# Performance work log

Hardware: AMD Instinct MI355X
Metric: run time of the kernel (lower is better)

The kernel has to match this reference:

```python
import jax, jax.numpy as jnp
import numpy as np

B, T, H, DD, DS = 256, 365, 512, 32, 27  # batch, timesteps, units, num_dynamic, num_static


def setup_inputs() -> dict:
    key = jax.random.key(0)
    ks = jax.random.split(key, 6)
    scale = 0.05
    bias = jnp.zeros((3 * H,), jnp.float32).at[:H].add(1.0)  # unit forget bias on f-block
    return {
        "x_dyn": jax.random.normal(ks[0], (B, T, DD), jnp.float32),
        "x_static": jax.random.normal(ks[1], (B, DS), jnp.float32),
        "kernel": jax.random.normal(ks[2], (DD, 3 * H), jnp.float32) * scale,
        "recurrent_kernel": jax.random.normal(ks[3], (H, 3 * H), jnp.float32) * scale,
        "bias": bias,
        "static_kernel": jax.random.normal(ks[4], (DS, H), jnp.float32) * scale,
        "static_bias": jnp.zeros((H,), jnp.float32),
    }


def hard_sigmoid(x):
    return jnp.clip(0.2 * x + 0.5, 0.0, 1.0)


def reference(x_dyn, x_static, kernel, recurrent_kernel, bias, static_kernel, static_bias):
    Hn = static_bias.shape[0]
    # static input gate, constant across time: [B, H]
    i_gate = hard_sigmoid(x_static @ static_kernel + static_bias)
    # precompute input contribution for all timesteps: [T, B, 3H]
    zx = jnp.einsum('btd,dk->tbk', x_dyn, kernel) + bias

    def step(carry, z_t):
        h, c = carry
        z = z_t + h @ recurrent_kernel  # [B, 3H]
        f = hard_sigmoid(z[:, :Hn])
        g = jnp.tanh(z[:, Hn:2 * Hn])
        o = hard_sigmoid(z[:, 2 * Hn:])
        c = f * c + i_gate * g
        h = o * jnp.tanh(c)
        return (h, c), h

    b = x_dyn.shape[0]
    h0 = jnp.zeros((b, Hn), x_dyn.dtype)
    (_, _), hs = jax.lax.scan(step, (h0, h0), zx)
    return jnp.transpose(hs, (1, 0, 2))  # [B, T, H]
```

## Files before the change

### kernel.cpp

```cpp
#include <hip/hip_runtime.h>
#include <stdint.h>

#define TSTEPS 365
#define BATCH  256
#define HU     512
#define DDIM   32
#define DSTAT  27
#define KTOT   544
#define KPAD   552
#define NCOLS  96
#define ZPAD   20

typedef __attribute__((ext_vector_type(8))) short s8v;
typedef __attribute__((ext_vector_type(4))) float f4v;

__device__ __forceinline__ float b2f(uint16_t u) {
    union { uint32_t i; float f; } v; v.i = ((uint32_t)u) << 16; return v.f;
}
__device__ __forceinline__ uint16_t f2b(float f) {
    uint32_t x = __float_as_uint(f);
    uint32_t r = x + 0x7FFFu + ((x >> 16) & 1u);
    return (uint16_t)(r >> 16);
}
__device__ __forceinline__ float loadf(const void* p, long i, bool fp32) {
    return fp32 ? ((const float*)p)[i] : b2f(((const uint16_t*)p)[i]);
}
__device__ __forceinline__ bool detect_fp32(const void* bias) {
    return *((const uint32_t*)bias) == 0x3F800000u;
}
__device__ __forceinline__ float hsig(float x) {
    return fminf(fmaxf(0.2f * x + 0.5f, 0.0f), 1.0f);
}
__device__ __forceinline__ float tanh_fast(float x) {
    float e = __expf(2.0f * x);
    return 1.0f - 2.0f * __builtin_amdgcn_rcpf(e + 1.0f);
}
__device__ __forceinline__ uint32_t load_x_nt(const void* x, bool fp32, int b, int t, int d) {
    long i = ((long)b * TSTEPS + t) * DDIM + d;
    return fp32 ? __builtin_nontemporal_load(((const uint32_t*)x) + i)
                : (uint32_t)__builtin_nontemporal_load(((const uint16_t*)x) + i);
}
__device__ __forceinline__ float xval(uint32_t r, bool fp32) {
    return fp32 ? __uint_as_float(r) : b2f((uint16_t)r);
}

__global__ __launch_bounds__(256) void k_prep_w(
    const void* __restrict__ rk, const void* __restrict__ kin,
    const void* __restrict__ bias,
    uint16_t* __restrict__ Wc, float* __restrict__ biasf)
{
    bool fp32 = detect_fp32(bias);
    __shared__ float tile[32][33];
    int jt = blockIdx.x, kt = blockIdx.y;
    int c = threadIdx.x & 31, r0 = threadIdx.x >> 5;
    #pragma unroll
    for (int i = 0; i < 4; i++) {
        int r = r0 + 8 * i;
        int k = kt * 32 + r, j = jt * 32 + c;
        float v;
        if (k < HU) v = loadf(rk, (long)k * 1536 + j, fp32);
        else        v = loadf(kin, (long)(k - HU) * 1536 + j, fp32);
        tile[r][c] = v;
    }
    __syncthreads();
    #pragma unroll
    for (int i = 0; i < 4; i++) {
        int r = r0 + 8 * i;
        int j = jt * 32 + r, k = kt * 32 + c;
        Wc[(long)j * KTOT + k] = f2b(tile[c][r]);
    }
    if (jt == 0 && kt == 0)
        for (int idx = threadIdx.x; idx < 1536; idx += 256)
            biasf[idx] = loadf(bias, idx, fp32);
}

__global__ __launch_bounds__(256) void k_igate(
    const void* __restrict__ xs, const void* __restrict__ sk,
    const void* __restrict__ sbias, const void* __restrict__ bias,
    float* __restrict__ igate)
{
    bool fp32 = detect_fp32(bias);
    int b = blockIdx.x;
    for (int u = threadIdx.x; u < HU; u += 256) {
        float acc = loadf(sbias, u, fp32);
        #pragma unroll
        for (int d = 0; d < DSTAT; d++)
            acc += loadf(xs, (long)b * DSTAT + d, fp32) * loadf(sk, (long)d * HU + u, fp32);
        igate[(long)b * HU + u] = hsig(acc);
    }
}

__device__ __forceinline__ void unpack_h(uint64_t v, uint16_t* rowh, uint16_t* rowl, int u2) {
    uint32_t p0 = (uint32_t)v, p1 = (uint32_t)(v >> 32);
    *(uint32_t*)&rowh[u2] = (p0 >> 16) | (p1 & 0xFFFF0000u);
    *(uint32_t*)&rowl[u2] = (p0 & 0xFFFFu) | (p1 << 16);
}

__global__ __launch_bounds__(512) void k_persist(
    const void* __restrict__ xdyn, const void* __restrict__ bias,
    const uint16_t* __restrict__ Wc, const float* __restrict__ biasf,
    const float* __restrict__ igate,
    uint64_t* __restrict__ h0, uint64_t* __restrict__ h1,
    void* __restrict__ out)
{
    bool fp32 = detect_fp32(bias);
    __shared__ __align__(16) uint16_t ldsAh[16][KPAD];
    __shared__ __align__(16) uint16_t ldsAl[16][KPAD];
    __shared__ __align__(16) float    zbufP[2][NCOLS][ZPAD];

    int tid = threadIdx.x;
    int bg = blockIdx.x & 15;
    int ug = blockIdx.x >> 4;
    int wv = tid >> 6, lane = tid & 63;
    int n = lane & 15, q = lane >> 4;
    int gte = wv >> 1, hh = wv & 1;

    s8v wr0[9], wr1[9];
    float bz0 = 0.f, bz1 = 0.f;
    if (wv < 6) {
        int j0 = (gte << 9) + (ug << 5) + n;
        int j1 = j0 + 16;
        if (hh == 0) {
            #pragma unroll
            for (int kk = 0; kk < 9; kk++) {
                int k0 = kk * 32 + q * 8;
                wr0[kk] = *(const s8v*)(Wc + (long)j0 * KTOT + k0);
                wr1[kk] = *(const s8v*)(Wc + (long)j1 * KTOT + k0);
            }
            bz0 = biasf[j0];
            bz1 = biasf[j1];
        } else {
            #pragma unroll
            for (int kk = 0; kk < 8; kk++) {
                int k0 = (9 + kk) * 32 + q * 8;
                wr0[kk] = *(const s8v*)(Wc + (long)j0 * KTOT + k0);
                wr1[kk] = *(const s8v*)(Wc + (long)j1 * KTOT + k0);
            }
        }
    }

    int em = tid >> 5;
    int sl = tid & 31;
    int eb = bg * 16 + em;
    int ugb = ug << 5;
    float ig0 = igate[(long)eb * HU + ugb + sl];
    float c0r = 0.f;
    long rowbase = ((long)eb) << 8;

    for (int t = 0; t < TSTEPS; t++) {
        const uint64_t* Rp = (t & 1) ? h1 : h0;
        uint64_t*       Wp = (t & 1) ? h0 : h1;

        uint32_t xr0 = load_x_nt(xdyn, fp32, bg * 16 + em, t, sl);

        uint64_t hb[8];
        if (t == 0) {
            #pragma unroll
            for (int i = 0; i < 8; i++) hb[i] = 0ull;
        } else {
            uint32_t texp = (((uint32_t)(t - 1)) >> 1) & 1u;
            int guard = 0;
            for (;;) {
                #pragma unroll
                for (int i = 0; i < 8; i++)
                    hb[i] = __hip_atomic_load(&Rp[rowbase + i * 32 + sl],
                                              __ATOMIC_RELAXED, __HIP_MEMORY_SCOPE_AGENT);
                uint32_t bad = 0;
                #pragma unroll
                for (int i = 0; i < 8; i++)
                    bad |= ((uint32_t)hb[i] ^ texp) & 1u;
                if (__all((int)(bad == 0))) break;
                if (++guard > (1 << 20)) break;
                if (guard > 64) __builtin_amdgcn_s_sleep(1);
            }
            asm volatile("" ::: "memory");
        }
        #pragma unroll
        for (int i = 0; i < 8; i++)
            unpack_h(hb[i], ldsAh[em], ldsAl[em], 2 * (i * 32 + sl));

        {
            float v0 = xval(xr0, fp32);
            uint16_t a0 = f2b(v0);
            ldsAh[em][HU + sl] = a0;
            ldsAl[em][HU + sl] = f2b(v0 - b2f(a0));
        }
        __syncthreads();

        if (wv < 6) {
            f4v a0h, a1h;
            if (hh == 0) { a0h = (f4v){bz0, bz0, bz0, bz0}; a1h = (f4v){bz1, bz1, bz1, bz1}; }
            else         { a0h = (f4v){0.f, 0.f, 0.f, 0.f}; a1h = (f4v){0.f, 0.f, 0.f, 0.f}; }
            f4v a0l = {0.f, 0.f, 0.f, 0.f}, a1l = {0.f, 0.f, 0.f, 0.f};
            if (hh == 0) {
                #pragma unroll
                for (int kk = 0; kk < 9; kk++) {
                    int k0 = kk * 32 + q * 8;
                    s8v ah = *(const s8v*)&ldsAh[n][k0];
                    s8v al = *(const s8v*)&ldsAl[n][k0];
                    a0h = __builtin_amdgcn_mfma_f32_16x16x32_bf16(ah, wr0[kk], a0h, 0, 0, 0);
                    a1h = __builtin_amdgcn_mfma_f32_16x16x32_bf16(ah, wr1[kk], a1h, 0, 0, 0);
                    a0l = __builtin_amdgcn_mfma_f32_16x16x32_bf16(al, wr0[kk], a0l, 0, 0, 0);
                    a1l = __builtin_amdgcn_mfma_f32_16x16x32_bf16(al, wr1[kk], a1l, 0, 0, 0);
                }
            } else {
                #pragma unroll
                for (int kk = 0; kk < 8; kk++) {
                    int k0 = (9 + kk) * 32 + q * 8;
                    s8v ah = *(const s8v*)&ldsAh[n][k0];
                    s8v al = *(const s8v*)&ldsAl[n][k0];
                    a0h = __builtin_amdgcn_mfma_f32_16x16x32_bf16(ah, wr0[kk], a0h, 0, 0, 0);
                    a1h = __builtin_amdgcn_mfma_f32_16x16x32_bf16(ah, wr1[kk], a1h, 0, 0, 0);
                    a0l = __builtin_amdgcn_mfma_f32_16x16x32_bf16(al, wr0[kk], a0l, 0, 0, 0);
                    a1l = __builtin_amdgcn_mfma_f32_16x16x32_bf16(al, wr1[kk], a1l, 0, 0, 0);
                }
            }
            int ci0 = (gte << 5) + n, ci1 = ci0 + 16;
            *(f4v*)&zbufP[hh][ci0][q * 4] = a0h + a0l;
            *(f4v*)&zbufP[hh][ci1][q * 4] = a1h + a1l;
        }
        __syncthreads();

        {
            float zf = zbufP[0][sl][em]      + zbufP[1][sl][em];
            float zg = zbufP[0][32 + sl][em] + zbufP[1][32 + sl][em];
            float zo = zbufP[0][64 + sl][em] + zbufP[1][64 + sl][em];
            float f0 = hsig(zf);
            float g0 = tanh_fast(zg);
            float o0 = hsig(zo);
            c0r = f0 * c0r + ig0 * g0;
            float hv0 = o0 * tanh_fast(c0r);
            uint32_t tg = (((uint32_t)t) >> 1) & 1u;
            uint16_t hi0 = f2b(hv0);
            uint16_t lo0 = (uint16_t)((f2b(hv0 - b2f(hi0)) & 0xFFFEu) | tg);
            uint32_t me32 = ((uint32_t)hi0 << 16) | lo0;
            uint32_t nb32 = __shfl_down(me32, 1);
            if (!(sl & 1)) {
                uint64_t pk = ((uint64_t)nb32 << 32) | me32;
                __hip_atomic_store(&Wp[rowbase + (ugb >> 1) + (sl >> 1)], pk,
                                   __ATOMIC_RELAXED, __HIP_MEMORY_SCOPE_AGENT);
            }
            long oo = ((long)eb * TSTEPS + t) * HU + ugb + sl;
            if (fp32) {
                __builtin_nontemporal_store(hv0, &((float*)out)[oo]);
            } else if (!(sl & 1)) {
                __builtin_nontemporal_store(
                    (uint32_t)(hi0 | (nb32 & 0xFFFF0000u)), &((uint32_t*)out)[oo >> 1]);
            }
        }
    }
}

__global__ __launch_bounds__(256) void k_step_fb(
    const void* __restrict__ xdyn, const void* __restrict__ bias,
    const uint16_t* __restrict__ Wc, const float* __restrict__ biasf,
    const float* __restrict__ igate, float* __restrict__ c_fb,
    const uint64_t* __restrict__ Rp, uint64_t* __restrict__ Wp,
    void* __restrict__ out, int t)
{
    bool fp32 = detect_fp32(bias);
    __shared__ __align__(16) uint16_t ldsAh[16][KPAD];
    __shared__ __align__(16) uint16_t ldsAl[16][KPAD];
    __shared__ __align__(16) float    zbuf[NCOLS][ZPAD];

    int tid = threadIdx.x;
    int bg = blockIdx.x & 15;
    int ug = blockIdx.x >> 4;
    int w = tid >> 6, lane = tid & 63;
    int n = lane & 15, q = lane >> 4;
    int em = tid >> 4, ep = tid & 15;
    int u0 = 2 * ep, u1 = u0 + 1;
    int eb = bg * 16 + em;
    int ugb = ug << 5;

    long rowbase = ((long)eb) << 8;
    #pragma unroll 4
    for (int kb = 0; kb < 16; kb++)
        unpack_h((t == 0) ? 0ull : Rp[rowbase + kb * 16 + ep],
                 ldsAh[em], ldsAl[em], kb * 32 + 2 * ep);
    #pragma unroll
    for (int it = 0; it < 2; it++) {
        int e = tid + it * 256;
        int m = e >> 5, d = e & 31;
        float v = loadf(xdyn, ((long)(bg * 16 + m) * TSTEPS + t) * DDIM + d, fp32);
        uint16_t hi = f2b(v);
        ldsAh[m][HU + d] = hi;
        ldsAl[m][HU + d] = f2b(v - b2f(hi));
    }
    __syncthreads();

    if (w < 3) {
        int j0 = (w << 9) + (ug << 5) + n;
        int j1 = j0 + 16;
        float bz0 = biasf[j0], bz1 = biasf[j1];
        f4v a0h = {bz0, bz0, bz0, bz0}, a0l = {0.f, 0.f, 0.f, 0.f};
        f4v a1h = {bz1, bz1, bz1, bz1}, a1l = {0.f, 0.f, 0.f, 0.f};
        #pragma unroll
        for (int kt = 0; kt < 17; kt++) {
            int k0 = kt * 32 + q * 8;
            s8v b0 = *(const s8v*)(Wc + (long)j0 * KTOT + k0);
            s8v b1 = *(const s8v*)(Wc + (long)j1 * KTOT + k0);
            s8v ah = *(const s8v*)&ldsAh[n][k0];
            s8v al = *(const s8v*)&ldsAl[n][k0];
            a0h = __builtin_amdgcn_mfma_f32_16x16x32_bf16(ah, b0, a0h, 0, 0, 0);
            a1h = __builtin_amdgcn_mfma_f32_16x16x32_bf16(ah, b1, a1h, 0, 0, 0);
            a0l = __builtin_amdgcn_mfma_f32_16x16x32_bf16(al, b0, a0l, 0, 0, 0);
            a1l = __builtin_amdgcn_mfma_f32_16x16x32_bf16(al, b1, a1l, 0, 0, 0);
        }
        int ci0 = 32 * w + n, ci1 = ci0 + 16;
        *(f4v*)&zbuf[ci0][q * 4] = a0h + a0l;
        *(f4v*)&zbuf[ci1][q * 4] = a1h + a1l;
    }
    __syncthreads();

    {
        float f0 = hsig(zbuf[u0][em]);
        float g0 = tanhf(zbuf[32 + u0][em]);
        float o0 = hsig(zbuf[64 + u0][em]);
        float f1 = hsig(zbuf[u1][em]);
        float g1 = tanhf(zbuf[32 + u1][em]);
        float o1 = hsig(zbuf[64 + u1][em]);
        float2* cp = (float2*)&c_fb[((long)eb << 9) + ugb + u0];
        float2 cv = *cp;
        cv.x = f0 * cv.x + igate[(long)eb * HU + ugb + u0] * g0;
        cv.y = f1 * cv.y + igate[(long)eb * HU + ugb + u1] * g1;
        *cp = cv;
        float hv0 = o0 * tanhf(cv.x);
        float hv1 = o1 * tanhf(cv.y);
        uint16_t hi0 = f2b(hv0), lo0 = f2b(hv0 - b2f(hi0));
        uint16_t hi1 = f2b(hv1), lo1 = f2b(hv1 - b2f(hi1));
        Wp[((long)eb << 8) + (ugb >> 1) + ep] =
            ((uint64_t)(((uint32_t)hi1 << 16) | lo1) << 32) | (((uint32_t)hi0 << 16) | lo0);
        long oo = ((long)eb * TSTEPS + t) * HU + ugb + u0;
        if (fp32) {
            ((float*)out)[oo] = hv0;
            ((float*)out)[oo + 1] = hv1;
        } else {
            ((uint32_t*)out)[oo >> 1] = hi0 | ((uint32_t)hi1 << 16);
        }
    }
}

extern "C" void kernel_launch(void* const* d_in, const int* in_sizes, int n_in,
                              void* d_out, int out_size, void* d_ws, size_t ws_size,
                              hipStream_t stream) {
    const void* xdyn  = d_in[0];
    const void* xstat = d_in[1];
    const void* kin   = d_in[2];
    const void* rk    = d_in[3];
    const void* bias  = d_in[4];
    const void* sk    = d_in[5];
    const void* sbias = d_in[6];

    char* w = (char*)d_ws;
    size_t off = 0;
    uint16_t* Wc = (uint16_t*)(w + off);  off += (size_t)1536 * KTOT * 2;
    float* biasf = (float*)(w + off);     off += 1536 * 4;
    float* igate = (float*)(w + off);     off += (size_t)BATCH * HU * 4;
    size_t hs = off;
    uint64_t* h0 = (uint64_t*)(w + off);  off += (size_t)BATCH * HU * 2 * 2;
    uint64_t* h1 = (uint64_t*)(w + off);  off += (size_t)BATCH * HU * 2 * 2;
    size_t he = off;
    float* c_fb  = (float*)(w + off);     off += (size_t)BATCH * HU * 4;

    hipMemsetAsync(w + hs, 0x01, he - hs, stream);
    hipMemsetAsync(w + he, 0, off - he, stream);

    k_prep_w<<<dim3(48, 17), 256, 0, stream>>>(rk, kin, bias, Wc, biasf);
    k_igate<<<dim3(256), 256, 0, stream>>>(xstat, sk, sbias, bias, igate);

    void* args[] = {
        (void*)&xdyn, (void*)&bias, (void*)&Wc, (void*)&biasf, (void*)&igate,
        (void*)&h0, (void*)&h1, (void*)&d_out
    };
    hipError_t err = hipLaunchCooperativeKernel((void*)k_persist, dim3(256), dim3(512),
                                                args, 0, stream);
    if (err != hipSuccess) {
        for (int t = 0; t < TSTEPS; t++) {
            const uint64_t* Rp = (t & 1) ? h1 : h0;
            uint64_t* Wp = (t & 1) ? h0 : h1;
            k_step_fb<<<dim3(256), 256, 0, stream>>>(xdyn, bias, Wc, biasf, igate,
                                                     c_fb, Rp, Wp, d_out, t);
        }
    }
    (void)ws_size; (void)n_in; (void)out_size; (void)in_sizes;
}
```

Baseline: 1.105 ms.

## Double block size to 1024 threads, splitting MFMA columns across twice the waves

The persistent LSTM kernel now launches 1024-thread blocks. Each of 12 waves computes one 16-column MFMA tile instead of two, which halves the serial MFMA chain per wave. The h-vector polling load is spread over all 16 waves, so each lane reads 4 words instead of 8. The cost is more waves contending in each __syncthreads, only half the threads doing the elementwise update, and a tighter register budget under launch_bounds(1024).

```diff
diff --git a/kernel.cpp b/kernel.cpp
--- a/kernel.cpp
+++ b/kernel.cpp
@@ -96,7 +96,7 @@
     *(uint32_t*)&rowl[u2] = (p0 & 0xFFFFu) | (p1 << 16);
 }
 
-__global__ __launch_bounds__(512) void k_persist(
+__global__ __launch_bounds__(1024, 4) void k_persist(
     const void* __restrict__ xdyn, const void* __restrict__ bias,
     const uint16_t* __restrict__ Wc, const float* __restrict__ biasf,
     const float* __restrict__ igate,
@@ -113,61 +113,56 @@
     int ug = blockIdx.x >> 4;
     int wv = tid >> 6, lane = tid & 63;
     int n = lane & 15, q = lane >> 4;
-    int gte = wv >> 1, hh = wv & 1;
-
-    s8v wr0[9], wr1[9];
-    float bz0 = 0.f, bz1 = 0.f;
-    if (wv < 6) {
-        int j0 = (gte << 9) + (ug << 5) + n;
-        int j1 = j0 + 16;
+    int gte = wv >> 2, hh = (wv >> 1) & 1, js = wv & 1;
+
+    s8v wr0[9];
+    float bz0 = 0.f;
+    if (wv < 12) {
+        int j0 = (gte << 9) + (ug << 5) + (js << 4) + n;
         if (hh == 0) {
             #pragma unroll
-            for (int kk = 0; kk < 9; kk++) {
-                int k0 = kk * 32 + q * 8;
-                wr0[kk] = *(const s8v*)(Wc + (long)j0 * KTOT + k0);
-                wr1[kk] = *(const s8v*)(Wc + (long)j1 * KTOT + k0);
-            }
+            for (int kk = 0; kk < 9; kk++)
+                wr0[kk] = *(const s8v*)(Wc + (long)j0 * KTOT + kk * 32 + q * 8);
             bz0 = biasf[j0];
-            bz1 = biasf[j1];
         } else {
             #pragma unroll
-            for (int kk = 0; kk < 8; kk++) {
-                int k0 = (9 + kk) * 32 + q * 8;
-                wr0[kk] = *(const s8v*)(Wc + (long)j0 * KTOT + k0);
-                wr1[kk] = *(const s8v*)(Wc + (long)j1 * KTOT + k0);
-            }
-        }
-    }
-
-    int em = tid >> 5;
-    int sl = tid & 31;
-    int eb = bg * 16 + em;
+            for (int kk = 0; kk < 8; kk++)
+                wr0[kk] = *(const s8v*)(Wc + (long)j0 * KTOT + (9 + kk) * 32 + q * 8);
+        }
+    }
+
+    int grow = wv;
+    long growbase = ((long)(bg * 16 + grow)) << 8;
+
+    int em = tid >> 5, sl = tid & 31;
     int ugb = ug << 5;
-    float ig0 = igate[(long)eb * HU + ugb + sl];
-    float c0r = 0.f;
+    int eb = bg * 16 + (em & 15);
+    float ig0 = 0.f, c0r = 0.f;
+    if (tid < 512) ig0 = igate[(long)eb * HU + ugb + sl];
     long rowbase = ((long)eb) << 8;
 
     for (int t = 0; t < TSTEPS; t++) {
         const uint64_t* Rp = (t & 1) ? h1 : h0;
         uint64_t*       Wp = (t & 1) ? h0 : h1;
 
-        uint32_t xr0 = load_x_nt(xdyn, fp32, bg * 16 + em, t, sl);
-
-        uint64_t hb[8];
+        uint32_t xr0 = 0;
+        if (tid < 512) xr0 = load_x_nt(xdyn, fp32, eb, t, sl);
+
+        uint64_t hb[4];
         if (t == 0) {
             #pragma unroll
-            for (int i = 0; i < 8; i++) hb[i] = 0ull;
+            for (int i = 0; i < 4; i++) hb[i] = 0ull;
         } else {
             uint32_t texp = (((uint32_t)(t - 1)) >> 1) & 1u;
             int guard = 0;
             for (;;) {
                 #pragma unroll
-                for (int i = 0; i < 8; i++)
-                    hb[i] = __hip_atomic_load(&Rp[rowbase + i * 32 + sl],
+                for (int i = 0; i < 4; i++)
+                    hb[i] = __hip_atomic_load(&Rp[growbase + i * 64 + lane],
                                               __ATOMIC_RELAXED, __HIP_MEMORY_SCOPE_AGENT);
                 uint32_t bad = 0;
                 #pragma unroll
-                for (int i = 0; i < 8; i++)
+                for (int i = 0; i < 4; i++)
                     bad |= ((uint32_t)hb[i] ^ texp) & 1u;
                 if (__all((int)(bad == 0))) break;
                 if (++guard > (1 << 20)) break;
@@ -176,10 +171,10 @@
             asm volatile("" ::: "memory");
         }
         #pragma unroll
-        for (int i = 0; i < 8; i++)
-            unpack_h(hb[i], ldsAh[em], ldsAl[em], 2 * (i * 32 + sl));
-
-        {
+        for (int i = 0; i < 4; i++)
+            unpack_h(hb[i], ldsAh[grow], ldsAl[grow], 2 * (i * 64 + lane));
+
+        if (tid < 512) {
             float v0 = xval(xr0, fp32);
             uint16_t a0 = f2b(v0);
             ldsAh[em][HU + sl] = a0;
@@ -187,11 +182,9 @@
         }
         __syncthreads();
 
-        if (wv < 6) {
-            f4v a0h, a1h;
-            if (hh == 0) { a0h = (f4v){bz0, bz0, bz0, bz0}; a1h = (f4v){bz1, bz1, bz1, bz1}; }
-            else         { a0h = (f4v){0.f, 0.f, 0.f, 0.f}; a1h = (f4v){0.f, 0.f, 0.f, 0.f}; }
-            f4v a0l = {0.f, 0.f, 0.f, 0.f}, a1l = {0.f, 0.f, 0.f, 0.f};
+        if (wv < 12) {
+            f4v a0h = (hh == 0) ? (f4v){bz0, bz0, bz0, bz0} : (f4v){0.f, 0.f, 0.f, 0.f};
+            f4v a0l = {0.f, 0.f, 0.f, 0.f};
             if (hh == 0) {
                 #pragma unroll
                 for (int kk = 0; kk < 9; kk++) {
@@ -199,9 +192,7 @@
                     s8v ah = *(const s8v*)&ldsAh[n][k0];
                     s8v al = *(const s8v*)&ldsAl[n][k0];
                     a0h = __builtin_amdgcn_mfma_f32_16x16x32_bf16(ah, wr0[kk], a0h, 0, 0, 0);
-                    a1h = __builtin_amdgcn_mfma_f32_16x16x32_bf16(ah, wr1[kk], a1h, 0, 0, 0);
                     a0l = __builtin_amdgcn_mfma_f32_16x16x32_bf16(al, wr0[kk], a0l, 0, 0, 0);
-                    a1l = __builtin_amdgcn_mfma_f32_16x16x32_bf16(al, wr1[kk], a1l, 0, 0, 0);
                 }
             } else {
                 #pragma unroll
@@ -210,18 +201,15 @@
                     s8v ah = *(const s8v*)&ldsAh[n][k0];
                     s8v al = *(const s8v*)&ldsAl[n][k0];
                     a0h = __builtin_amdgcn_mfma_f32_16x16x32_bf16(ah, wr0[kk], a0h, 0, 0, 0);
-                    a1h = __builtin_amdgcn_mfma_f32_16x16x32_bf16(ah, wr1[kk], a1h, 0, 0, 0);
                     a0l = __builtin_amdgcn_mfma_f32_16x16x32_bf16(al, wr0[kk], a0l, 0, 0, 0);
-                    a1l = __builtin_amdgcn_mfma_f32_16x16x32_bf16(al, wr1[kk], a1l, 0, 0, 0);
                 }
             }
-            int ci0 = (gte << 5) + n, ci1 = ci0 + 16;
-            *(f4v*)&zbufP[hh][ci0][q * 4] = a0h + a0l;
-            *(f4v*)&zbufP[hh][ci1][q * 4] = a1h + a1l;
+            int ci = (gte << 5) + (js << 4) + n;
+            *(f4v*)&zbufP[hh][ci][q * 4] = a0h + a0l;
         }
         __syncthreads();
 
-        {
+        if (tid < 512) {
             float zf = zbufP[0][sl][em]      + zbufP[1][sl][em];
             float zg = zbufP[0][32 + sl][em] + zbufP[1][32 + sl][em];
             float zo = zbufP[0][64 + sl][em] + zbufP[1][64 + sl][em];
@@ -373,7 +361,7 @@
         (void*)&xdyn, (void*)&bias, (void*)&Wc, (void*)&biasf, (void*)&igate,
         (void*)&h0, (void*)&h1, (void*)&d_out
     };
-    hipError_t err = hipLaunchCooperativeKernel((void*)k_persist, dim3(256), dim3(512),
+    hipError_t err = hipLaunchCooperativeKernel((void*)k_persist, dim3(256), dim3(1024),
                                                 args, 0, stream);
     if (err != hipSuccess) {
         for (int t = 0; t < TSTEPS; t++) {
```

Measured after the change: 1.490 ms. 34.9% more time.
